# Kernel tuning notes

Measured on AMD Instinct MI355X. Metric: run time of the kernel, lower is better.

Reference implementation:

```python
import jax, jax.numpy as jnp
import numpy as np

BATCH, SEQ, H, P, N, L = 8, 8192, 16, 64, 64, 64  # batch, seq, heads, d_head, d_state, block_len


def setup_inputs() -> dict:
    key = jax.random.key(0)
    k1, k2, k3 = jax.random.split(key, 3)
    X = jax.random.normal(k1, (BATCH, SEQ, H, P), dtype=jnp.float32)
    # A is the log-decay; scale down so exp(cumsum) stays finite over 8192 steps
    A = jax.random.normal(k2, (BATCH, SEQ, H), dtype=jnp.float32) * 0.02
    B = jax.random.normal(k3, (BATCH, SEQ, H, N), dtype=jnp.float32)
    return {"X": X, "A": A, "B": B}


def reference(X, A, B):
    b, s, h, p = X.shape
    n = B.shape[-1]
    l = L
    c = s // l  # n_chunks

    Xb = X.reshape(b, c, l, h, p)                      # (b,c,l,h,p)
    Ab = A.reshape(b, c, l, h).transpose(0, 3, 1, 2)   # (b,h,c,l)
    Bb = B.reshape(b, c, l, h, n)                      # (b,c,l,h,n)

    # intra-chunk cumulative decay
    A_cs = jnp.cumsum(Ab, axis=-1)                     # (b,h,c,l)
    decay_states = jnp.exp(A_cs[..., -1:] - A_cs)      # (b,h,c,l)

    # per-chunk state: sum_l decay * B outer X -> (b,c,h,p,n)
    states = jnp.einsum('bhcl,bclhn,bclhp->bchpn', decay_states, Bb, Xb)

    # prepend zero initial state
    init = jnp.zeros((b, 1, h, p, n), dtype=X.dtype)
    all_states = jnp.concatenate([init, states], axis=1)  # (b,c+1,h,p,n)

    # cross-chunk decay-weighted combination into final state
    A_ends = A_cs[..., -1]                                # (b,h,c)
    A_pad_cs = jnp.cumsum(jnp.pad(A_ends, ((0, 0), (0, 0), (1, 0))), axis=-1)  # (b,h,c+1)
    decay_chunk = jnp.exp(A_pad_cs[..., -1:] - A_pad_cs)  # (b,h,c+1)

    final_states = jnp.einsum('bhc,bchpn->bhpn', decay_chunk, all_states)  # (b,h,p,n)
    return final_states
```

## Files before the change

### kernel.cpp

```cpp
#include <hip/hip_runtime.h>

#define BATCH 8
#define SEQ   8192
#define NH    16
#define DP    64
#define ROWF  (NH*DP)
#define HGRP  4
#define NTHR  512
#define KT    32
#define RS    260

typedef __attribute__((ext_vector_type(8))) short bf16x8;
typedef __attribute__((ext_vector_type(4))) float f32x4;

static __device__ __forceinline__ unsigned pk2(float lo, float hi) {
    unsigned a = __builtin_bit_cast(unsigned, lo);
    unsigned b = __builtin_bit_cast(unsigned, hi);
    a = (a + 0x7FFFu + ((a >> 16) & 1u)) >> 16;
    b = (b + 0x7FFFu + ((b >> 16) & 1u)) & 0xFFFF0000u;
    return (a & 0xFFFFu) | b;
}

template<int NBLK>
__global__ __launch_bounds__(NTHR)
void k_partial(const float* __restrict__ Xg, const float* __restrict__ Ag,
               const float* __restrict__ Bg, float* __restrict__ part,
               float* __restrict__ blockA)
{
    constexpr int TB  = SEQ / NBLK;
    constexpr int Q   = TB / 64;
    constexpr int NKT = TB / KT;

    __shared__ unsigned XL[2][16][RS];
    __shared__ unsigned BL[2][16][RS];
    __shared__ float    WT[HGRP][TB];

    const int gid  = blockIdx.x;
    const int blk  = gid % NBLK;
    const int hg   = (gid / NBLK) & 3;
    const int b    = gid / (4 * NBLK);
    const int tid  = threadIdx.x;
    const int w    = tid >> 6;
    const int lane = tid & 63;
    const int hloc = w >> 1;
    const int nh   = w & 1;
    const int h    = hg * HGRP + hloc;
    const int t0   = blk * TB;

    float c[Q];
    {
        const size_t abase = ((size_t)(b * SEQ + t0 + lane * Q)) * NH + h;
        float run = 0.f;
        #pragma unroll
        for (int k = 0; k < Q; ++k) { run += Ag[abase + (size_t)k * NH]; c[k] = run; }
    }
    float tsum = c[Q - 1], s = tsum;
    #pragma unroll
    for (int d = 1; d < 64; d <<= 1) {
        float o = __shfl_up(s, d, 64);
        if (lane >= d) s += o;
    }
    const float total = __shfl(s, 63, 64);
    const float excl  = s - tsum;
    if (nh == 0) {
        #pragma unroll
        for (int k = 0; k < Q; ++k)
            WT[hloc][lane * Q + k] = __expf(total - (excl + c[k]));
        if (lane == 63) blockA[(size_t)(b * NH + h) * NBLK + blk] = total;
    }

    f32x4 acc[4][2];
    #pragma unroll
    for (int mi = 0; mi < 4; ++mi)
        #pragma unroll
        for (int ni = 0; ni < 2; ++ni) acc[mi][ni] = (f32x4){0.f, 0.f, 0.f, 0.f};

    const int hl = lane >> 4;
    const int p4 = (lane & 15) * 4;
    const size_t gbase = (size_t)(b * SEQ + t0) * ROWF + hg * (HGRP * DP) + hl * DP + p4;

    auto issue = [&](int k, float4* lx, float4* lb) {
        if (k >= NKT) return;
        const size_t tb = gbase + (size_t)(k * KT + w * 4) * ROWF;
        #pragma unroll
        for (int i = 0; i < 4; ++i) {
            lx[i] = *(const float4*)(Xg + tb + (size_t)i * ROWF);
            lb[i] = *(const float4*)(Bg + tb + (size_t)i * ROWF);
        }
    };
    auto cwrite = [&](int k, int buf, const float4* lx, const float4* lb) {
        const int tIn = k * KT + w * 4;
        #pragma unroll
        for (int q = 0; q < 2; ++q) {
            const float w0 = WT[hl][tIn + 2 * q];
            const float w1 = WT[hl][tIn + 2 * q + 1];
            const int   tp = w * 2 + q;
            const float* x0 = (const float*)&lx[2 * q];
            const float* x1 = (const float*)&lx[2 * q + 1];
            const float* b0 = (const float*)&lb[2 * q];
            const float* b1 = (const float*)&lb[2 * q + 1];
            #pragma unroll
            for (int pp = 0; pp < 4; ++pp) {
                XL[buf][tp][hl * 64 + p4 + pp] = pk2(x0[pp] * w0, x1[pp] * w1);
                BL[buf][tp][hl * 64 + p4 + pp] = pk2(b0[pp], b1[pp]);
            }
        }
    };
    auto compute = [&](int buf) {
        const int r  = lane & 15;
        const int kg = lane >> 4;
        uint4 af[4], bf[2];
        #pragma unroll
        for (int mi = 0; mi < 4; ++mi) {
            const int row = hloc * 64 + mi * 16 + r;
            af[mi].x = XL[buf][kg * 4 + 0][row];
            af[mi].y = XL[buf][kg * 4 + 1][row];
            af[mi].z = XL[buf][kg * 4 + 2][row];
            af[mi].w = XL[buf][kg * 4 + 3][row];
        }
        #pragma unroll
        for (int ni = 0; ni < 2; ++ni) {
            const int row = hloc * 64 + nh * 32 + ni * 16 + r;
            bf[ni].x = BL[buf][kg * 4 + 0][row];
            bf[ni].y = BL[buf][kg * 4 + 1][row];
            bf[ni].z = BL[buf][kg * 4 + 2][row];
            bf[ni].w = BL[buf][kg * 4 + 3][row];
        }
        #pragma unroll
        for (int mi = 0; mi < 4; ++mi) {
            const bf16x8 a = __builtin_bit_cast(bf16x8, af[mi]);
            #pragma unroll
            for (int ni = 0; ni < 2; ++ni) {
                const bf16x8 bb = __builtin_bit_cast(bf16x8, bf[ni]);
                acc[mi][ni] = __builtin_amdgcn_mfma_f32_16x16x32_bf16(
                                  a, bb, acc[mi][ni], 0, 0, 0);
            }
        }
    };

    float4 sx0[4], sb0[4], sx1[4], sb1[4];
    issue(0, sx0, sb0);
    issue(1, sx1, sb1);
    __syncthreads();

    cwrite(0, 0, sx0, sb0);
    issue(2, sx0, sb0);
    asm volatile("s_waitcnt lgkmcnt(0)" ::: "memory");
    __builtin_amdgcn_s_barrier();
    __builtin_amdgcn_sched_barrier(0);

    #pragma unroll 1
    for (int k = 0; k < NKT; k += 2) {
        if (k + 1 < NKT) { cwrite(k + 1, 1, sx1, sb1); issue(k + 3, sx1, sb1); }
        compute(0);
        asm volatile("s_waitcnt lgkmcnt(0)" ::: "memory");
        __builtin_amdgcn_s_barrier();
        __builtin_amdgcn_sched_barrier(0);

        if (k + 2 < NKT) { cwrite(k + 2, 0, sx0, sb0); issue(k + 4, sx0, sb0); }
        if (k + 1 < NKT) compute(1);
        asm volatile("s_waitcnt lgkmcnt(0)" ::: "memory");
        __builtin_amdgcn_s_barrier();
        __builtin_amdgcn_sched_barrier(0);
    }

    float* dst = part + ((size_t)(b * NH + h) * NBLK + blk) * 4096;
    {
        const int r  = lane & 15;
        const int cg = lane >> 4;
        #pragma unroll
        for (int mi = 0; mi < 4; ++mi)
            #pragma unroll
            for (int ni = 0; ni < 2; ++ni)
                #pragma unroll
                for (int rr = 0; rr < 4; ++rr)
                    dst[(mi * 16 + cg * 4 + rr) * 64 + nh * 32 + ni * 16 + r] =
                        acc[mi][ni][rr];
    }
}

__global__ void k_scales(const float* __restrict__ blockA, float* __restrict__ scale,
                         int nblk)
{
    const int bh = blockIdx.x * blockDim.x + threadIdx.x;
    if (bh < BATCH * NH) {
        float run = 0.f;
        for (int c2 = nblk - 1; c2 >= 0; --c2) {
            scale[bh * nblk + c2] = __expf(run);
            run += blockA[bh * nblk + c2];
        }
    }
}

__global__ __launch_bounds__(256)
void k_combine(const float* __restrict__ part, const float* __restrict__ scale,
               float* __restrict__ out, int nblk)
{
    const int idx = blockIdx.x * 256 + threadIdx.x;
    const int bh  = idx >> 12;
    const int e   = idx & 4095;
    float r = 0.f;
    for (int q = 0; q < nblk; ++q)
        r += scale[bh * nblk + q] * part[((size_t)bh * nblk + q) * 4096 + e];
    out[idx] = r;
}

extern "C" void kernel_launch(void* const* d_in, const int* in_sizes, int n_in,
                              void* d_out, int out_size, void* d_ws, size_t ws_size,
                              hipStream_t stream)
{
    const float* X = (const float*)d_in[0];
    const float* A = (const float*)d_in[1];
    const float* B = (const float*)d_in[2];
    float* out     = (float*)d_out;

    const size_t need32 = ((size_t)BATCH * NH * 32 * 4096 + 2ull * BATCH * NH * 32) * 4;
    const int nblk = (ws_size >= need32) ? 32 : 16;

    float* part   = (float*)d_ws;
    float* blockA = part + (size_t)BATCH * NH * nblk * 4096;
    float* scale  = blockA + (size_t)BATCH * NH * nblk;

    if (nblk == 32)
        hipLaunchKernelGGL((k_partial<32>), dim3(BATCH * 4 * 32), dim3(NTHR), 0, stream,
                           X, A, B, part, blockA);
    else
        hipLaunchKernelGGL((k_partial<16>), dim3(BATCH * 4 * 16), dim3(NTHR), 0, stream,
                           X, A, B, part, blockA);

    hipLaunchKernelGGL(k_scales, dim3(1), dim3(128), 0, stream, blockA, scale, nblk);
    hipLaunchKernelGGL(k_combine, dim3((BATCH * NH * 4096) / 256), dim3(256), 0, stream,
                       part, scale, out, nblk);
}
```

Measured before the change: 145.5 us.

## Deepen global prefetch to three stages and vectorize LDS stores in partial kernel

For the 32-block configuration, the K-loop is fully unrolled into eight steps with three register staging buffers, so global loads run two tiles ahead instead of one. Separately, the bf16-packed LDS writes for X and B now go out as single 128-bit stores instead of four scalar stores. Both aim to hide global memory latency and cut LDS store instruction count. The price is more VGPRs spent on staging, which may lower occupancy or cause spills. RS=260 keeps the 16-byte stores aligned.

```diff
diff --git a/kernel.cpp b/kernel.cpp
--- a/kernel.cpp
+++ b/kernel.cpp
@@ -99,11 +99,17 @@
             const float* x1 = (const float*)&lx[2 * q + 1];
             const float* b0 = (const float*)&lb[2 * q];
             const float* b1 = (const float*)&lb[2 * q + 1];
-            #pragma unroll
-            for (int pp = 0; pp < 4; ++pp) {
-                XL[buf][tp][hl * 64 + p4 + pp] = pk2(x0[pp] * w0, x1[pp] * w1);
-                BL[buf][tp][hl * 64 + p4 + pp] = pk2(b0[pp], b1[pp]);
-            }
+            uint4 xv, bv;
+            xv.x = pk2(x0[0] * w0, x1[0] * w1);
+            xv.y = pk2(x0[1] * w0, x1[1] * w1);
+            xv.z = pk2(x0[2] * w0, x1[2] * w1);
+            xv.w = pk2(x0[3] * w0, x1[3] * w1);
+            bv.x = pk2(b0[0], b1[0]);
+            bv.y = pk2(b0[1], b1[1]);
+            bv.z = pk2(b0[2], b1[2]);
+            bv.w = pk2(b0[3], b1[3]);
+            *(uint4*)&XL[buf][tp][hl * 64 + p4] = xv;
+            *(uint4*)&BL[buf][tp][hl * 64 + p4] = bv;
         }
     };
     auto compute = [&](int buf) {
@@ -138,31 +144,43 @@
         }
     };
 
-    float4 sx0[4], sb0[4], sx1[4], sb1[4];
-    issue(0, sx0, sb0);
-    issue(1, sx1, sb1);
-    __syncthreads();
-
-    cwrite(0, 0, sx0, sb0);
-    issue(2, sx0, sb0);
-    asm volatile("s_waitcnt lgkmcnt(0)" ::: "memory");
-    __builtin_amdgcn_s_barrier();
-    __builtin_amdgcn_sched_barrier(0);
-
-    #pragma unroll 1
-    for (int k = 0; k < NKT; k += 2) {
-        if (k + 1 < NKT) { cwrite(k + 1, 1, sx1, sb1); issue(k + 3, sx1, sb1); }
-        compute(0);
-        asm volatile("s_waitcnt lgkmcnt(0)" ::: "memory");
-        __builtin_amdgcn_s_barrier();
-        __builtin_amdgcn_sched_barrier(0);
-
-        if (k + 2 < NKT) { cwrite(k + 2, 0, sx0, sb0); issue(k + 4, sx0, sb0); }
-        if (k + 1 < NKT) compute(1);
-        asm volatile("s_waitcnt lgkmcnt(0)" ::: "memory");
-        __builtin_amdgcn_s_barrier();
-        __builtin_amdgcn_sched_barrier(0);
-    }
+    #define PHASE_BAR() do { \
+        asm volatile("s_waitcnt lgkmcnt(0)" ::: "memory"); \
+        __builtin_amdgcn_s_barrier(); \
+        __builtin_amdgcn_sched_barrier(0); } while (0)
+
+    if constexpr (NBLK == 32) {
+        float4 s0x[4], s0b[4], s1x[4], s1b[4], s2x[4], s2b[4];
+        issue(0, s0x, s0b);
+        issue(1, s1x, s1b);
+        issue(2, s2x, s2b);
+        __syncthreads();
+
+        cwrite(0, 0, s0x, s0b); issue(3, s0x, s0b); PHASE_BAR();
+        cwrite(1, 1, s1x, s1b); issue(4, s1x, s1b); compute(0); PHASE_BAR();
+        cwrite(2, 0, s2x, s2b); issue(5, s2x, s2b); compute(1); PHASE_BAR();
+        cwrite(3, 1, s0x, s0b); issue(6, s0x, s0b); compute(0); PHASE_BAR();
+        cwrite(4, 0, s1x, s1b); issue(7, s1x, s1b); compute(1); PHASE_BAR();
+        cwrite(5, 1, s2x, s2b);                     compute(0); PHASE_BAR();
+        cwrite(6, 0, s0x, s0b);                     compute(1); PHASE_BAR();
+        cwrite(7, 1, s1x, s1b);                     compute(0); PHASE_BAR();
+        compute(1);
+    } else {
+        float4 sx0[4], sb0[4], sx1[4], sb1[4];
+        issue(0, sx0, sb0);
+        issue(1, sx1, sb1);
+        __syncthreads();
+        cwrite(0, 0, sx0, sb0); issue(2, sx0, sb0); PHASE_BAR();
+        #pragma unroll 1
+        for (int k = 0; k < NKT; k += 2) {
+            if (k + 1 < NKT) { cwrite(k + 1, 1, sx1, sb1); issue(k + 3, sx1, sb1); }
+            compute(0); PHASE_BAR();
+            if (k + 2 < NKT) { cwrite(k + 2, 0, sx0, sb0); issue(k + 4, sx0, sb0); }
+            if (k + 1 < NKT) compute(1);
+            PHASE_BAR();
+        }
+    }
+    #undef PHASE_BAR
 
     float* dst = part + ((size_t)(b * NH + h) * NBLK + blk) * 4096;
     {
```

Result: no change. 143.9 us (-1.1%).

## Double K tile, restructure load pipeline, vectorize LDS writes, fold scale kernel into combine

Applied to the files above, without the earlier changes.

Doubles the K tile to 64 timesteps per stage so each barrier covers two MFMA k-halves, which halves the number of barriers. The pipeline now prefetches in half-tiles with a single buffer swap per iteration. LDS stores of packed bf16 become 128-bit vector writes, and launch bounds request two blocks per CU. The separate serial k_scales kernel is removed, and k_combine now computes the exponential decay scales inline, saving one launch at the cost of redundant exp work per element and a larger LDS footprint.

```diff
diff --git a/kernel.cpp b/kernel.cpp
--- a/kernel.cpp
+++ b/kernel.cpp
@@ -7,7 +7,7 @@
 #define ROWF  (NH*DP)
 #define HGRP  4
 #define NTHR  512
-#define KT    32
+#define KT    64
 #define RS    260
 
 typedef __attribute__((ext_vector_type(8))) short bf16x8;
@@ -22,7 +22,7 @@
 }
 
 template<int NBLK>
-__global__ __launch_bounds__(NTHR)
+__global__ __launch_bounds__(NTHR, 2)
 void k_partial(const float* __restrict__ Xg, const float* __restrict__ Ag,
                const float* __restrict__ Bg, float* __restrict__ part,
                float* __restrict__ blockA)
@@ -31,8 +31,8 @@
     constexpr int Q   = TB / 64;
     constexpr int NKT = TB / KT;
 
-    __shared__ unsigned XL[2][16][RS];
-    __shared__ unsigned BL[2][16][RS];
+    __shared__ unsigned XL[2][32][RS];
+    __shared__ unsigned BL[2][32][RS];
     __shared__ float    WT[HGRP][TB];
 
     const int gid  = blockIdx.x;
@@ -79,89 +79,86 @@
     const int p4 = (lane & 15) * 4;
     const size_t gbase = (size_t)(b * SEQ + t0) * ROWF + hg * (HGRP * DP) + hl * DP + p4;
 
-    auto issue = [&](int k, float4* lx, float4* lb) {
+    auto issueH = [&](int k, int half, float4* lx, float4* lb) {
         if (k >= NKT) return;
-        const size_t tb = gbase + (size_t)(k * KT + w * 4) * ROWF;
+        const size_t tb = gbase + (size_t)(k * KT + w * 8 + half * 4) * ROWF;
         #pragma unroll
         for (int i = 0; i < 4; ++i) {
             lx[i] = *(const float4*)(Xg + tb + (size_t)i * ROWF);
             lb[i] = *(const float4*)(Bg + tb + (size_t)i * ROWF);
         }
     };
-    auto cwrite = [&](int k, int buf, const float4* lx, const float4* lb) {
-        const int tIn = k * KT + w * 4;
-        #pragma unroll
-        for (int q = 0; q < 2; ++q) {
-            const float w0 = WT[hl][tIn + 2 * q];
-            const float w1 = WT[hl][tIn + 2 * q + 1];
-            const int   tp = w * 2 + q;
-            const float* x0 = (const float*)&lx[2 * q];
-            const float* x1 = (const float*)&lx[2 * q + 1];
-            const float* b0 = (const float*)&lb[2 * q];
-            const float* b1 = (const float*)&lb[2 * q + 1];
-            #pragma unroll
-            for (int pp = 0; pp < 4; ++pp) {
-                XL[buf][tp][hl * 64 + p4 + pp] = pk2(x0[pp] * w0, x1[pp] * w1);
-                BL[buf][tp][hl * 64 + p4 + pp] = pk2(b0[pp], b1[pp]);
-            }
+    auto cwriteH = [&](int k, int buf, int half, const float4* lx, const float4* lb) {
+        const int tBase = k * KT + w * 8 + half * 4;
+        #pragma unroll
+        for (int q2 = 0; q2 < 2; ++q2) {
+            const float w0 = WT[hl][tBase + 2 * q2];
+            const float w1 = WT[hl][tBase + 2 * q2 + 1];
+            const int   tp = w * 4 + half * 2 + q2;
+            const float* x0 = (const float*)&lx[2 * q2];
+            const float* x1 = (const float*)&lx[2 * q2 + 1];
+            const float* b0 = (const float*)&lb[2 * q2];
+            const float* b1 = (const float*)&lb[2 * q2 + 1];
+            uint4 xv, bv;
+            xv.x = pk2(x0[0] * w0, x1[0] * w1);
+            xv.y = pk2(x0[1] * w0, x1[1] * w1);
+            xv.z = pk2(x0[2] * w0, x1[2] * w1);
+            xv.w = pk2(x0[3] * w0, x1[3] * w1);
+            bv.x = pk2(b0[0], b1[0]);
+            bv.y = pk2(b0[1], b1[1]);
+            bv.z = pk2(b0[2], b1[2]);
+            bv.w = pk2(b0[3], b1[3]);
+            *(uint4*)&XL[buf][tp][hl * 64 + p4] = xv;
+            *(uint4*)&BL[buf][tp][hl * 64 + p4] = bv;
         }
     };
-    auto compute = [&](int buf) {
+    auto computeKH = [&](int buf, int kh) {
         const int r  = lane & 15;
         const int kg = lane >> 4;
         uint4 af[4], bf[2];
         #pragma unroll
         for (int mi = 0; mi < 4; ++mi) {
             const int row = hloc * 64 + mi * 16 + r;
-            af[mi].x = XL[buf][kg * 4 + 0][row];
-            af[mi].y = XL[buf][kg * 4 + 1][row];
-            af[mi].z = XL[buf][kg * 4 + 2][row];
-            af[mi].w = XL[buf][kg * 4 + 3][row];
+            af[mi].x = XL[buf][kh * 16 + kg * 4 + 0][row];
+            af[mi].y = XL[buf][kh * 16 + kg * 4 + 1][row];
+            af[mi].z = XL[buf][kh * 16 + kg * 4 + 2][row];
+            af[mi].w = XL[buf][kh * 16 + kg * 4 + 3][row];
         }
         #pragma unroll
         for (int ni = 0; ni < 2; ++ni) {
             const int row = hloc * 64 + nh * 32 + ni * 16 + r;
-            bf[ni].x = BL[buf][kg * 4 + 0][row];
-            bf[ni].y = BL[buf][kg * 4 + 1][row];
-            bf[ni].z = BL[buf][kg * 4 + 2][row];
-            bf[ni].w = BL[buf][kg * 4 + 3][row];
+            bf[ni].x = BL[buf][kh * 16 + kg * 4 + 0][row];
+            bf[ni].y = BL[buf][kh * 16 + kg * 4 + 1][row];
+            bf[ni].z = BL[buf][kh * 16 + kg * 4 + 2][row];
+            bf[ni].w = BL[buf][kh * 16 + kg * 4 + 3][row];
         }
         #pragma unroll
         for (int mi = 0; mi < 4; ++mi) {
             const bf16x8 a = __builtin_bit_cast(bf16x8, af[mi]);
             #pragma unroll
-            for (int ni = 0; ni < 2; ++ni) {
-                const bf16x8 bb = __builtin_bit_cast(bf16x8, bf[ni]);
+            for (int ni = 0; ni < 2; ++ni)
                 acc[mi][ni] = __builtin_amdgcn_mfma_f32_16x16x32_bf16(
-                                  a, bb, acc[mi][ni], 0, 0, 0);
-            }
+                                  a, __builtin_bit_cast(bf16x8, bf[ni]),
+                                  acc[mi][ni], 0, 0, 0);
         }
     };
 
-    float4 sx0[4], sb0[4], sx1[4], sb1[4];
-    issue(0, sx0, sb0);
-    issue(1, sx1, sb1);
+    float4 h0x[4], h0b[4], h1x[4], h1b[4];
     __syncthreads();
-
-    cwrite(0, 0, sx0, sb0);
-    issue(2, sx0, sb0);
-    asm volatile("s_waitcnt lgkmcnt(0)" ::: "memory");
-    __builtin_amdgcn_s_barrier();
-    __builtin_amdgcn_sched_barrier(0);
+    issueH(0, 0, h0x, h0b);
 
     #pragma unroll 1
-    for (int k = 0; k < NKT; k += 2) {
-        if (k + 1 < NKT) { cwrite(k + 1, 1, sx1, sb1); issue(k + 3, sx1, sb1); }
-        compute(0);
+    for (int k = 0; k < NKT; ++k) {
+        const int buf = k & 1;
+        issueH(k, 1, h1x, h1b);
+        cwriteH(k, buf, 0, h0x, h0b);
+        issueH(k + 1, 0, h0x, h0b);
+        cwriteH(k, buf, 1, h1x, h1b);
         asm volatile("s_waitcnt lgkmcnt(0)" ::: "memory");
         __builtin_amdgcn_s_barrier();
         __builtin_amdgcn_sched_barrier(0);
-
-        if (k + 2 < NKT) { cwrite(k + 2, 0, sx0, sb0); issue(k + 4, sx0, sb0); }
-        if (k + 1 < NKT) compute(1);
-        asm volatile("s_waitcnt lgkmcnt(0)" ::: "memory");
-        __builtin_amdgcn_s_barrier();
-        __builtin_amdgcn_sched_barrier(0);
+        computeKH(buf, 0);
+        computeKH(buf, 1);
     }
 
     float* dst = part + ((size_t)(b * NH + h) * NBLK + blk) * 4096;
@@ -179,29 +176,18 @@
     }
 }
 
-__global__ void k_scales(const float* __restrict__ blockA, float* __restrict__ scale,
-                         int nblk)
-{
-    const int bh = blockIdx.x * blockDim.x + threadIdx.x;
-    if (bh < BATCH * NH) {
-        float run = 0.f;
-        for (int c2 = nblk - 1; c2 >= 0; --c2) {
-            scale[bh * nblk + c2] = __expf(run);
-            run += blockA[bh * nblk + c2];
-        }
-    }
-}
-
 __global__ __launch_bounds__(256)
-void k_combine(const float* __restrict__ part, const float* __restrict__ scale,
+void k_combine(const float* __restrict__ part, const float* __restrict__ blockA,
                float* __restrict__ out, int nblk)
 {
     const int idx = blockIdx.x * 256 + threadIdx.x;
     const int bh  = idx >> 12;
     const int e   = idx & 4095;
-    float r = 0.f;
-    for (int q = 0; q < nblk; ++q)
-        r += scale[bh * nblk + q] * part[((size_t)bh * nblk + q) * 4096 + e];
+    float r = 0.f, run = 0.f;
+    for (int q = nblk - 1; q >= 0; --q) {
+        r   += __expf(run) * part[((size_t)bh * nblk + q) * 4096 + e];
+        run += blockA[bh * nblk + q];
+    }
     out[idx] = r;
 }
 
@@ -214,12 +200,11 @@
     const float* B = (const float*)d_in[2];
     float* out     = (float*)d_out;
 
-    const size_t need32 = ((size_t)BATCH * NH * 32 * 4096 + 2ull * BATCH * NH * 32) * 4;
+    const size_t need32 = ((size_t)BATCH * NH * 32 * 4096 + (size_t)BATCH * NH * 32) * 4;
     const int nblk = (ws_size >= need32) ? 32 : 16;
 
     float* part   = (float*)d_ws;
     float* blockA = part + (size_t)BATCH * NH * nblk * 4096;
-    float* scale  = blockA + (size_t)BATCH * NH * nblk;
 
     if (nblk == 32)
         hipLaunchKernelGGL((k_partial<32>), dim3(BATCH * 4 * 32), dim3(NTHR), 0, stream,
@@ -228,7 +213,6 @@
         hipLaunchKernelGGL((k_partial<16>), dim3(BATCH * 4 * 16), dim3(NTHR), 0, stream,
                            X, A, B, part, blockA);
 
-    hipLaunchKernelGGL(k_scales, dim3(1), dim3(128), 0, stream, blockA, scale, nblk);
     hipLaunchKernelGGL(k_combine, dim3((BATCH * NH * 4096) / 256), dim3(256), 0, stream,
-                       part, scale, out, nblk);
-}
+                       part, blockA, out, nblk);
+}
```

Result: slower. 156.8 us (+7.8%).
